# Kernel tuning notes

Measured on AMD Instinct MI355X. Metric: run time of the kernel, lower is better.

Reference implementation:

```python
import jax, jax.numpy as jnp
import numpy as np

N_NODES = 50000
N_EDGES = 800000
D = 64
LN_EPS = 1e-5


def setup_inputs() -> dict:
    key = jax.random.key(0)
    k1, k2, k3 = jax.random.split(key, 3)
    x = jax.random.normal(k1, (N_NODES, D), dtype=jnp.float32)
    edge_index = jax.random.randint(k2, (2, N_EDGES), 0, N_NODES, dtype=jnp.int64)
    # GCNConv linear weight (no bias in lin; conv bias separate), kaiming-ish scale
    W = jax.random.normal(k3, (D, D), dtype=jnp.float32) / np.sqrt(D)
    b = jnp.zeros((D,), dtype=jnp.float32)
    # LayerNorm affine params
    gamma = jnp.ones((D,), dtype=jnp.float32)
    beta = jnp.zeros((D,), dtype=jnp.float32)
    return {"x": x, "edge_index": edge_index, "W": W, "b": b, "gamma": gamma, "beta": beta}


def reference(x, edge_index, W, b, gamma, beta):
    n = x.shape[0]
    # --- GCNConv (normalize=True, improved=False, add_self_loops=True) ---
    loops = jnp.arange(n, dtype=edge_index.dtype)
    src = jnp.concatenate([edge_index[0], loops])  # message sources j
    dst = jnp.concatenate([edge_index[1], loops])  # message targets i
    ew = jnp.ones(src.shape[0], dtype=x.dtype)
    deg = jax.ops.segment_sum(ew, dst, num_segments=n)          # in-degree incl. self-loop
    dinv = jnp.where(deg > 0, jax.lax.rsqrt(jnp.where(deg > 0, deg, 1.0)), 0.0)
    norm = dinv[src] * dinv[dst]                                 # [E+N]
    xw = x @ W                                                   # [N, D]
    z = jax.ops.segment_sum(norm[:, None] * xw[src], dst, num_segments=n) + b
    # --- identity skip connection ---
    h = x + z
    # --- norm_act_drop: LayerNorm + ReLU (dropout_prob=0) ---
    mu = jnp.mean(h, axis=-1, keepdims=True)
    var = jnp.mean((h - mu) ** 2, axis=-1, keepdims=True)
    hn = (h - mu) * jax.lax.rsqrt(var + LN_EPS)
    return jax.nn.relu(hn * gamma + beta)
```

## Files before the change

kernel.cpp:

```cpp
#include <hip/hip_runtime.h>
#include <hip/hip_fp16.h>

#define N_NODES 50000
#define N_EDGES 800000
#define D 64
#define LN_EPS 1e-5f
#define CAP 48
#define SENT 50000
#define NR 8
#define RSPAN ((N_NODES + NR - 1) / NR)
#define CPB 1024
#define NCH ((N_EDGES / 4 + CPB - 1) / CPB)
#define PREP_NB ((N_EDGES / 4 + 255) / 256)
#define GEMM_NB ((N_NODES + 63) / 64)
#define CNT_PAD 50048
#define XS_ROWS 50008

typedef unsigned short u16;
typedef unsigned int u32;


__global__ __launch_bounds__(256) void prep_gemm_k(const int* __restrict__ src,
                                                   const int* __restrict__ dst,
                                                   u32* __restrict__ pe,
                                                   int* __restrict__ cnt,
                                                   const float* __restrict__ x,
                                                   const float* __restrict__ W,
                                                   __half* __restrict__ xs) {
    __shared__ float xlds[D * D];
    int bid = blockIdx.x;
    int tid = threadIdx.x;
    if (bid < PREP_NB) {
        int gid = bid * 256 + tid;
        if (gid < CNT_PAD) cnt[gid] = 0;
        if (gid < N_EDGES / 4) {
            int4 s = ((const int4*)src)[gid];
            int4 d = ((const int4*)dst)[gid];
            uint4 p;
            p.x = (u32)(u16)d.x | ((u32)(u16)s.x << 16);
            p.y = (u32)(u16)d.y | ((u32)(u16)s.y << 16);
            p.z = (u32)(u16)d.z | ((u32)(u16)s.z << 16);
            p.w = (u32)(u16)d.w | ((u32)(u16)s.w << 16);
            ((uint4*)pe)[gid] = p;
        }
    } else {
        int row0 = (bid - PREP_NB) * 64;
        const float4* xg = (const float4*)(x + (size_t)row0 * D);
        float4* xl4 = (float4*)xlds;
        for (int i = tid; i < D * D / 4; i += 256) {
            int grow = row0 + (i >> 4);
            xl4[i] = (grow < N_NODES) ? xg[i] : make_float4(0.f, 0.f, 0.f, 0.f);
        }
        int lane = tid & 63;
        float wcol[D];
#pragma unroll
        for (int k = 0; k < D; ++k) wcol[k] = W[k * D + lane];
        __syncthreads();
        int wv = tid >> 6;
        for (int rr = 0; rr < 16; ++rr) {
            int r = wv * 16 + rr;
            int grow = row0 + r;
            if (grow >= N_NODES + 1) break;
            const float4* xr = (const float4*)(xlds + r * D);
            float acc = 0.f;
#pragma unroll
            for (int k4 = 0; k4 < 16; ++k4) {
                float4 xv = xr[k4];
                acc += xv.x * wcol[k4 * 4 + 0];
                acc += xv.y * wcol[k4 * 4 + 1];
                acc += xv.z * wcol[k4 * 4 + 2];
                acc += xv.w * wcol[k4 * 4 + 3];
            }
            xs[(size_t)grow * D + lane] = __float2half(acc);
        }
    }
}

__global__ __launch_bounds__(256) void fill_k(const u32* __restrict__ pe,
                                              int* __restrict__ cnt,
                                              u16* __restrict__ ssrc) {
    int r = blockIdx.x & (NR - 1);
    int chunk = blockIdx.x >> 3;
    int lo = r * RSPAN;
    int hi = lo + RSPAN; if (hi > N_NODES) hi = N_NODES;

    const uint4* pe4 = (const uint4*)pe;
    int u0 = chunk * CPB + threadIdx.x;
    u32 pp[16];
#pragma unroll
    for (int j = 0; j < 4; ++j) {
        int ui = u0 + j * 256;
        uint4 p = (ui < N_EDGES / 4) ? pe4[ui] : make_uint4(~0u, ~0u, ~0u, ~0u);
        pp[j * 4 + 0] = p.x; pp[j * 4 + 1] = p.y;
        pp[j * 4 + 2] = p.z; pp[j * 4 + 3] = p.w;
    }

    int pos[16];
    u32 vm = 0;
#pragma unroll
    for (int k = 0; k < 16; ++k) {
        int t = pp[k] & 0xffffu;
        if (t >= lo && t < hi) { pos[k] = atomicAdd(&cnt[t], 1); vm |= (1u << k); }
    }
#pragma unroll
    for (int k = 0; k < 16; ++k) {
        if ((vm >> k) & 1u) {
            int t = pp[k] & 0xffffu;
            if (pos[k] < CAP) ssrc[(size_t)t * CAP + pos[k]] = (u16)(pp[k] >> 16);
        }
    }
}

__global__ __launch_bounds__(256) void scale_k(const int* __restrict__ cnt,
                                               __half* __restrict__ xs) {
    int gid = blockIdx.x * 256 + threadIdx.x;
    if (gid >= N_NODES * 8) return;
    int row = gid >> 3;
    float di = rsqrtf((float)cnt[row] + 1.0f);
    float4 raw = ((const float4*)xs)[gid];
    __half2* hp = (__half2*)&raw;
#pragma unroll
    for (int i = 0; i < 4; ++i) {
        float2 f = __half22float2(hp[i]);
        hp[i] = __floats2half2_rn(di * f.x, di * f.y);
    }
    ((float4*)xs)[gid] = raw;
}

__global__ __launch_bounds__(256) void agg_ln_k(
        const float* __restrict__ x, const __half* __restrict__ xs,
        const int* __restrict__ cnt, const u16* __restrict__ ssrc,
        const float* __restrict__ b, const float* __restrict__ gamma,
        const float* __restrict__ beta, float* __restrict__ out) {
    int row = blockIdx.x * 4 + (threadIdx.x >> 6);
    if (row >= N_NODES) return;
    int lane = threadIdx.x & 63;
    int sub = lane >> 3;
    int c8  = lane & 7;
    size_t base = (size_t)row * CAP;

    int dc = cnt[row];
    int s0 = ssrc[base + sub + 0];
    int s1 = ssrc[base + sub + 8];
    int s2 = ssrc[base + sub + 16];
    int s3 = ssrc[base + sub + 24];
    int s4 = ssrc[base + sub + 32];
    int s5 = ssrc[base + sub + 40];
    const float4* xp = (const float4*)(x + (size_t)row * D + c8 * 8);
    float4 x0 = xp[0], x1 = xp[1];
    float4 xsr = make_float4(0.f, 0.f, 0.f, 0.f);
    if (sub == 0) xsr = *(const float4*)(xs + (size_t)row * D + c8 * 8);

    int deg = dc < CAP ? dc : CAP;
    int ns = (deg + 7) >> 3;

    int v0 = (sub +  0 < deg) ? s0 : SENT;
    int v1 = (sub +  8 < deg) ? s1 : SENT;
    int v2 = (sub + 16 < deg) ? s2 : SENT;
    int v3 = (sub + 24 < deg) ? s3 : SENT;
    int v4 = (sub + 32 < deg) ? s4 : SENT;
    int v5 = (sub + 40 < deg) ? s5 : SENT;

    float4 r0 = make_float4(0.f,0.f,0.f,0.f), r1 = r0, r2 = r0,
           r3 = r0, r4 = r0, r5 = r0;
    if (0 < ns) r0 = *(const float4*)(xs + (size_t)v0 * D + c8 * 8);
    if (1 < ns) r1 = *(const float4*)(xs + (size_t)v1 * D + c8 * 8);
    if (2 < ns) r2 = *(const float4*)(xs + (size_t)v2 * D + c8 * 8);
    if (3 < ns) r3 = *(const float4*)(xs + (size_t)v3 * D + c8 * 8);
    if (4 < ns) r4 = *(const float4*)(xs + (size_t)v4 * D + c8 * 8);
    if (5 < ns) r5 = *(const float4*)(xs + (size_t)v5 * D + c8 * 8);

    float di = rsqrtf((float)dc + 1.0f);

    float4 a0 = make_float4(0.f, 0.f, 0.f, 0.f);
    float4 a1 = make_float4(0.f, 0.f, 0.f, 0.f);
    {
        float4 rr[7] = {r0, r1, r2, r3, r4, r5, xsr};
#pragma unroll
        for (int k = 0; k < 7; ++k) {
            const __half2* hp = (const __half2*)&rr[k];
            float2 p0 = __half22float2(hp[0]), p1 = __half22float2(hp[1]);
            float2 p2 = __half22float2(hp[2]), p3 = __half22float2(hp[3]);
            a0.x += p0.x; a0.y += p0.y; a0.z += p1.x; a0.w += p1.y;
            a1.x += p2.x; a1.y += p2.y; a1.z += p3.x; a1.w += p3.y;
        }
    }

#pragma unroll
    for (int o = 8; o < 64; o <<= 1) {
        a0.x += __shfl_xor(a0.x, o, 64); a0.y += __shfl_xor(a0.y, o, 64);
        a0.z += __shfl_xor(a0.z, o, 64); a0.w += __shfl_xor(a0.w, o, 64);
        a1.x += __shfl_xor(a1.x, o, 64); a1.y += __shfl_xor(a1.y, o, 64);
        a1.z += __shfl_xor(a1.z, o, 64); a1.w += __shfl_xor(a1.w, o, 64);
    }

    const float4* bp = (const float4*)(b + c8 * 8);
    float4 b0 = bp[0], b1 = bp[1];

    float h[8];
    h[0] = x0.x + di * a0.x + b0.x;
    h[1] = x0.y + di * a0.y + b0.y;
    h[2] = x0.z + di * a0.z + b0.z;
    h[3] = x0.w + di * a0.w + b0.w;
    h[4] = x1.x + di * a1.x + b1.x;
    h[5] = x1.y + di * a1.y + b1.y;
    h[6] = x1.z + di * a1.z + b1.z;
    h[7] = x1.w + di * a1.w + b1.w;

    float s_ = 0.f;
#pragma unroll
    for (int i = 0; i < 8; ++i) s_ += h[i];
#pragma unroll
    for (int o = 1; o < 64; o <<= 1) s_ += __shfl_xor(s_, o, 64);
    float mu = s_ * (1.0f / 512.0f);
    float v_ = 0.f;
    float dd[8];
#pragma unroll
    for (int i = 0; i < 8; ++i) { dd[i] = h[i] - mu; v_ += dd[i] * dd[i]; }
#pragma unroll
    for (int o = 1; o < 64; o <<= 1) v_ += __shfl_xor(v_, o, 64);
    float rstd = rsqrtf(v_ * (1.0f / 512.0f) + LN_EPS);

    if (sub == 0) {
        const float4* gp = (const float4*)(gamma + c8 * 8);
        const float4* ep = (const float4*)(beta + c8 * 8);
        float4 g0 = gp[0], g1 = gp[1];
        float4 e0 = ep[0], e1 = ep[1];
        float4 w0, w1;
        w0.x = fmaxf(dd[0] * rstd * g0.x + e0.x, 0.f);
        w0.y = fmaxf(dd[1] * rstd * g0.y + e0.y, 0.f);
        w0.z = fmaxf(dd[2] * rstd * g0.z + e0.z, 0.f);
        w0.w = fmaxf(dd[3] * rstd * g0.w + e0.w, 0.f);
        w1.x = fmaxf(dd[4] * rstd * g1.x + e1.x, 0.f);
        w1.y = fmaxf(dd[5] * rstd * g1.y + e1.y, 0.f);
        w1.z = fmaxf(dd[6] * rstd * g1.z + e1.z, 0.f);
        w1.w = fmaxf(dd[7] * rstd * g1.w + e1.w, 0.f);
        float4* op = (float4*)(out + (size_t)row * D + c8 * 8);
        op[0] = w0;
        op[1] = w1;
    }
}

extern "C" void kernel_launch(void* const* d_in, const int* in_sizes, int n_in,
                              void* d_out, int out_size, void* d_ws, size_t ws_size,
                              hipStream_t stream) {
    const float* x     = (const float*)d_in[0];
    const int*   ei    = (const int*)d_in[1];
    const float* W     = (const float*)d_in[2];
    const float* b     = (const float*)d_in[3];
    const float* gamma = (const float*)d_in[4];
    const float* beta  = (const float*)d_in[5];
    float* out = (float*)d_out;

    const int* src = ei;
    const int* dst = ei + N_EDGES;

    int*    cnt  = (int*)d_ws;
    __half* xs   = (__half*)(cnt + CNT_PAD);
    u32*    pe   = (u32*)(xs + (size_t)XS_ROWS * D);
    u16*    ssrc = (u16*)(pe + N_EDGES);

    prep_gemm_k<<<PREP_NB + GEMM_NB, 256, 0, stream>>>(src, dst, pe, cnt, x, W, xs);
    fill_k<<<NR * NCH, 256, 0, stream>>>(pe, cnt, ssrc);
    scale_k<<<(N_NODES * 8 + 255) / 256, 256, 0, stream>>>(cnt, xs);
    agg_ln_k<<<(N_NODES + 3) / 4, 256, 0, stream>>>(x, xs, cnt, ssrc, b, gamma, beta, out);
}
```

Measured before the change: 163.5 us.

## Replace global-atomic CSR fill with LDS histogram, prefix scan, and scatter

Replaces the global-atomic fill kernel, which re-read all edges once per destination range, with a three-phase counting sort. First, per-chunk shared-memory histograms with packed 16-bit counters record each edge's local position. Next, a column-wise prefix scan over chunks builds per-chunk offsets and degree counts. Finally, a scatter pass writes sources into fixed-capacity slots, fused with the degree-scaling pass. This removes contended global atomics and redundant edge reads, at the cost of an extra launch, a large histogram buffer (98x50000 u16) and extra workspace traffic.

```diff
diff --git a/kernel.cpp b/kernel.cpp
--- a/kernel.cpp
+++ b/kernel.cpp
@@ -7,14 +7,14 @@
 #define LN_EPS 1e-5f
 #define CAP 48
 #define SENT 50000
-#define NR 8
-#define RSPAN ((N_NODES + NR - 1) / NR)
-#define CPB 1024
-#define NCH ((N_EDGES / 4 + CPB - 1) / CPB)
 #define PREP_NB ((N_EDGES / 4 + 255) / 256)
 #define GEMM_NB ((N_NODES + 63) / 64)
 #define CNT_PAD 50048
 #define XS_ROWS 50008
+#define NCHK 98
+#define CHSZ 8192
+#define HALF 25000
+#define SC_EB 782
 
 typedef unsigned short u16;
 typedef unsigned int u32;
@@ -23,7 +23,6 @@
 __global__ __launch_bounds__(256) void prep_gemm_k(const int* __restrict__ src,
                                                    const int* __restrict__ dst,
                                                    u32* __restrict__ pe,
-                                                   int* __restrict__ cnt,
                                                    const float* __restrict__ x,
                                                    const float* __restrict__ W,
                                                    __half* __restrict__ xs) {
@@ -32,7 +31,6 @@
     int tid = threadIdx.x;
     if (bid < PREP_NB) {
         int gid = bid * 256 + tid;
-        if (gid < CNT_PAD) cnt[gid] = 0;
         if (gid < N_EDGES / 4) {
             int4 s = ((const int4*)src)[gid];
             int4 d = ((const int4*)dst)[gid];
@@ -76,55 +74,103 @@
     }
 }
 
-__global__ __launch_bounds__(256) void fill_k(const u32* __restrict__ pe,
-                                              int* __restrict__ cnt,
-                                              u16* __restrict__ ssrc) {
-    int r = blockIdx.x & (NR - 1);
-    int chunk = blockIdx.x >> 3;
-    int lo = r * RSPAN;
-    int hi = lo + RSPAN; if (hi > N_NODES) hi = N_NODES;
-
-    const uint4* pe4 = (const uint4*)pe;
-    int u0 = chunk * CPB + threadIdx.x;
-    u32 pp[16];
-#pragma unroll
-    for (int j = 0; j < 4; ++j) {
-        int ui = u0 + j * 256;
-        uint4 p = (ui < N_EDGES / 4) ? pe4[ui] : make_uint4(~0u, ~0u, ~0u, ~0u);
-        pp[j * 4 + 0] = p.x; pp[j * 4 + 1] = p.y;
-        pp[j * 4 + 2] = p.z; pp[j * 4 + 3] = p.w;
-    }
-
-    int pos[16];
-    u32 vm = 0;
-#pragma unroll
-    for (int k = 0; k < 16; ++k) {
-        int t = pp[k] & 0xffffu;
-        if (t >= lo && t < hi) { pos[k] = atomicAdd(&cnt[t], 1); vm |= (1u << k); }
-    }
-#pragma unroll
-    for (int k = 0; k < 16; ++k) {
-        if ((vm >> k) & 1u) {
-            int t = pp[k] & 0xffffu;
-            if (pos[k] < CAP) ssrc[(size_t)t * CAP + pos[k]] = (u16)(pp[k] >> 16);
-        }
-    }
-}
-
-__global__ __launch_bounds__(256) void scale_k(const int* __restrict__ cnt,
-                                               __half* __restrict__ xs) {
-    int gid = blockIdx.x * 256 + threadIdx.x;
-    if (gid >= N_NODES * 8) return;
-    int row = gid >> 3;
-    float di = rsqrtf((float)cnt[row] + 1.0f);
-    float4 raw = ((const float4*)xs)[gid];
-    __half2* hp = (__half2*)&raw;
-#pragma unroll
-    for (int i = 0; i < 4; ++i) {
-        float2 f = __half22float2(hp[i]);
-        hp[i] = __floats2half2_rn(di * f.x, di * f.y);
-    }
-    ((float4*)xs)[gid] = raw;
+__global__ __launch_bounds__(256) void hist_k(const u32* __restrict__ pe,
+                                              u16* __restrict__ lpos,
+                                              u16* __restrict__ H) {
+    __shared__ u32 lh[HALF / 2];
+    int c = blockIdx.x >> 1;
+    int r = blockIdx.x & 1;
+    int rlo = r * HALF;
+    for (int w = threadIdx.x; w < HALF / 2; w += 256) lh[w] = 0;
+    __syncthreads();
+    int cbase = c * CHSZ;
+    u32* H32 = (u32*)H;
+#pragma unroll 4
+    for (int i = 0; i < CHSZ / 256; ++i) {
+        int e = cbase + threadIdx.x + i * 256;
+        if (e < N_EDGES) {
+            u32 p = pe[e];
+            int t = (int)(p & 0xffffu);
+            unsigned tr = (unsigned)(t - rlo);
+            if (tr < HALF) {
+                u32 addend = (tr & 1) ? 0x10000u : 1u;
+                u32 old = atomicAdd(&lh[tr >> 1], addend);
+                u32 lp = (tr & 1) ? (old >> 16) : (old & 0xffffu);
+                lpos[e] = (u16)lp;
+            }
+        }
+    }
+    __syncthreads();
+    for (int w = threadIdx.x; w < HALF / 2; w += 256)
+        H32[(size_t)c * (HALF) + r * (HALF / 2) + w] = lh[w];
+}
+
+__global__ __launch_bounds__(256) void pref_k(u16* __restrict__ H,
+                                              int* __restrict__ cnt) {
+    __shared__ u32 ph[NCHK * 128];
+    int n0 = blockIdx.x * 256;
+    int wbase = n0 >> 1;
+    u32* H32 = (u32*)H;
+    for (int idx = threadIdx.x; idx < NCHK * 128; idx += 256) {
+        int c = idx >> 7, w = idx & 127;
+        int gw = wbase + w;
+        ph[idx] = (gw < HALF) ? H32[(size_t)c * HALF + gw] : 0;
+    }
+    __syncthreads();
+    u16* ph16 = (u16*)ph;
+    u32 run = 0;
+    for (int c = 0; c < NCHK; ++c) {
+        int off = c * 256 + threadIdx.x;
+        u32 v = ph16[off];
+        ph16[off] = (u16)run;
+        run += v;
+    }
+    int n = n0 + threadIdx.x;
+    if (n < N_NODES) cnt[n] = (int)run;
+    __syncthreads();
+    for (int idx = threadIdx.x; idx < NCHK * 128; idx += 256) {
+        int c = idx >> 7, w = idx & 127;
+        int gw = wbase + w;
+        if (gw < HALF) H32[(size_t)c * HALF + gw] = ph[idx];
+    }
+}
+
+__global__ __launch_bounds__(256) void scatter_scale_k(const u32* __restrict__ pe,
+                                                       const u16* __restrict__ lpos,
+                                                       const u16* __restrict__ H,
+                                                       const int* __restrict__ cnt,
+                                                       u16* __restrict__ ssrc,
+                                                       __half* __restrict__ xs) {
+    int bid = blockIdx.x;
+    if (bid < SC_EB) {
+        int e4 = bid * 1024 + threadIdx.x * 4;
+        if (e4 >= N_EDGES) return;
+        uint4 p = ((const uint4*)pe)[e4 >> 2];
+        ushort4 lp = ((const ushort4*)lpos)[e4 >> 2];
+        int c = e4 >> 13;
+        const u16* st = H + (size_t)c * 50000;
+        u32 pp[4] = {p.x, p.y, p.z, p.w};
+        u16 ll[4] = {lp.x, lp.y, lp.z, lp.w};
+#pragma unroll
+        for (int k = 0; k < 4; ++k) {
+            int t = (int)(pp[k] & 0xffffu);
+            int pos = (int)st[t] + (int)ll[k];
+            if (pos < CAP) ssrc[(size_t)t * CAP + pos] = (u16)(pp[k] >> 16);
+        }
+    } else {
+        int gid = (bid - SC_EB) * 256 + threadIdx.x;
+        if (gid >= N_NODES * 8) return;
+        int row = gid >> 3;
+        float di = rsqrtf((float)cnt[row] + 1.0f);
+        float4 raw = ((const float4*)xs)[gid];
+        __half2* hp = (__half2*)&raw;
+#pragma unroll
+        for (int i = 0; i < 4; ++i) {
+            float2 f = __half22float2(hp[i]);
+            hp[i] = __floats2half2_rn(di * f.x, di * f.y);
+        }
+        ((float4*)xs)[gid] = raw;
+    }
 }
 
 __global__ __launch_bounds__(256) void agg_ln_k(
@@ -259,9 +305,13 @@
     __half* xs   = (__half*)(cnt + CNT_PAD);
     u32*    pe   = (u32*)(xs + (size_t)XS_ROWS * D);
     u16*    ssrc = (u16*)(pe + N_EDGES);
-
-    prep_gemm_k<<<PREP_NB + GEMM_NB, 256, 0, stream>>>(src, dst, pe, cnt, x, W, xs);
-    fill_k<<<NR * NCH, 256, 0, stream>>>(pe, cnt, ssrc);
-    scale_k<<<(N_NODES * 8 + 255) / 256, 256, 0, stream>>>(cnt, xs);
+    u16*    H    = ssrc + (size_t)N_NODES * CAP;
+    u16*    lpos = H + (size_t)NCHK * 50000;
+
+    prep_gemm_k<<<PREP_NB + GEMM_NB, 256, 0, stream>>>(src, dst, pe, x, W, xs);
+    hist_k<<<NCHK * 2, 256, 0, stream>>>(pe, lpos, H);
+    pref_k<<<(N_NODES + 255) / 256, 256, 0, stream>>>(H, cnt);
+    scatter_scale_k<<<SC_EB + (N_NODES * 8 + 255) / 256, 256, 0, stream>>>(
+        pe, lpos, H, cnt, ssrc, xs);
     agg_ln_k<<<(N_NODES + 3) / 4, 256, 0, stream>>>(x, xs, cnt, ssrc, b, gamma, beta, out);
 }
```

Measured after the change: 175.1 us. 7.1% more time.
